# Performance work log

Hardware: AMD Instinct MI355X
Metric: run time of the kernel (lower is better)

The kernel has to match this reference:

```python
import jax, jax.numpy as jnp
import numpy as np

# SMPL-style 22-joint kinematic tree; parents[i] < i for i >= 2 as the module's loop requires.
PARENTS = np.array([-1, 0, 0, 0, 1, 2, 3, 4, 5, 6, 7, 8, 9, 9, 9, 12, 13, 14, 16, 17, 18, 19])
L, J, D6 = 65536, 22, 6


def cont6d_to_mat(d6):
    """6D continuous rotation -> 3x3 rotation matrix (Gram-Schmidt). Columns are b1,b2,b3."""
    a1, a2 = d6[..., :3], d6[..., 3:]
    b1 = a1 / jnp.maximum(jnp.linalg.norm(a1, axis=-1, keepdims=True), 1e-12)
    b2 = a2 - b1 * jnp.sum(b1 * a2, axis=-1, keepdims=True)
    b2 = b2 / jnp.maximum(jnp.linalg.norm(b2, axis=-1, keepdims=True), 1e-12)
    b3 = jnp.cross(b1, b2)
    return jnp.stack((b1, b2, b3), axis=-1)  # (..., 3, 3)


def setup_inputs() -> dict:
    key = jax.random.key(0)
    k1, k2 = jax.random.split(key)
    pred_series = jax.random.normal(k1, (L, J, D6), dtype=jnp.float32)
    offsets = 0.1 * jax.random.normal(k2, (J, 3), dtype=jnp.float32)  # bone offsets (buffer)
    return {"pred_series": pred_series, "offsets": offsets}


def reference(pred_series, offsets):
    # pred_series: (L, 22, 6) -> global positions (L, 22, 3)
    rot_mats = cont6d_to_mat(pred_series)          # (L, 22, 3, 3)

    # Cumulative root rotation: R_t = R_{t-1} @ delta_t, R_{-1} = I  (sequential scan over time)
    deltas = rot_mats[:, 1]                        # (L, 3, 3)
    def step(R, d):
        Rn = R @ d
        return Rn, Rn
    _, R = jax.lax.scan(step, jnp.eye(3, dtype=pred_series.dtype), deltas)  # (L, 3, 3)

    # Root translation: integrate rotated local velocities
    vel_local = pred_series[:, 0, :3]              # (L, 3)
    global_vel = jnp.einsum('tij,tj->ti', R, vel_local)
    root_pos = jnp.cumsum(global_vel, axis=0)      # (L, 3)

    # FK down the static tree, vectorized over time; unrolled over 22 joints (static).
    rots = [None] * J
    pos = [None] * J
    rots[0], pos[0] = R, root_pos
    rots[1] = R
    pos[1] = pos[0] + jnp.einsum('tij,j->ti', R, offsets[1])
    for i in range(2, J):
        p = int(PARENTS[i])
        rots[i] = jnp.einsum('tij,tjk->tik', rots[p], rot_mats[:, i])
        pos[i] = pos[p] + jnp.einsum('tij,j->ti', rots[p], offsets[i])
    return jnp.stack(pos, axis=1)                  # (L, 22, 3)
```

## Files before the change

### kernel.cpp

```cpp
#include <hip/hip_runtime.h>
#include <stdint.h>


#define LTOT 65536
#define ROW 132
#define P1B 256
#define NBLK (LTOT / P1B)

struct Aff { float A[9]; float b[3]; };

__device__ __forceinline__ void d6_to_mat(float a0, float a1, float a2,
                                          float a3, float a4, float a5,
                                          float R[9]) {
  float n1 = sqrtf(a0 * a0 + a1 * a1 + a2 * a2);
  float i1 = 1.0f / fmaxf(n1, 1e-12f);
  float b10 = a0 * i1, b11 = a1 * i1, b12 = a2 * i1;
  float d = b10 * a3 + b11 * a4 + b12 * a5;
  float c0 = a3 - d * b10, c1 = a4 - d * b11, c2 = a5 - d * b12;
  float n2 = sqrtf(c0 * c0 + c1 * c1 + c2 * c2);
  float i2 = 1.0f / fmaxf(n2, 1e-12f);
  float b20 = c0 * i2, b21 = c1 * i2, b22 = c2 * i2;
  float b30 = b11 * b22 - b12 * b21;
  float b31 = b12 * b20 - b10 * b22;
  float b32 = b10 * b21 - b11 * b20;
  R[0] = b10; R[1] = b20; R[2] = b30;
  R[3] = b11; R[4] = b21; R[5] = b31;
  R[6] = b12; R[7] = b22; R[8] = b32;
}

__device__ __forceinline__ void mat_mul(const float A[9], const float B[9], float C[9]) {
#pragma unroll
  for (int i = 0; i < 3; ++i)
#pragma unroll
    for (int j = 0; j < 3; ++j)
      C[i * 3 + j] = A[i * 3 + 0] * B[0 + j] + A[i * 3 + 1] * B[3 + j] + A[i * 3 + 2] * B[6 + j];
}

__device__ __forceinline__ void mat_vec(const float A[9], float x, float y, float z,
                                        float& ox, float& oy, float& oz) {
  ox = A[0] * x + A[1] * y + A[2] * z;
  oy = A[3] * x + A[4] * y + A[5] * z;
  oz = A[6] * x + A[7] * y + A[8] * z;
}

__device__ __forceinline__ void compose(const Aff& P, const Aff& T, Aff& O) {
  mat_mul(P.A, T.A, O.A);
  float bx, by, bz;
  mat_vec(P.A, T.b[0], T.b[1], T.b[2], bx, by, bz);
  O.b[0] = P.b[0] + bx; O.b[1] = P.b[1] + by; O.b[2] = P.b[2] + bz;
}

__device__ __forceinline__ void aff_identity(Aff& v) {
  v.A[0] = 1.f; v.A[1] = 0.f; v.A[2] = 0.f;
  v.A[3] = 0.f; v.A[4] = 1.f; v.A[5] = 0.f;
  v.A[6] = 0.f; v.A[7] = 0.f; v.A[8] = 1.f;
  v.b[0] = 0.f; v.b[1] = 0.f; v.b[2] = 0.f;
}

__device__ __forceinline__ void wave_scan(Aff& v, int lane) {
#pragma unroll
  for (int s = 1; s < 64; s <<= 1) {
    Aff u;
#pragma unroll
    for (int k = 0; k < 9; ++k) u.A[k] = __shfl_up(v.A[k], s, 64);
#pragma unroll
    for (int k = 0; k < 3; ++k) u.b[k] = __shfl_up(v.b[k], s, 64);
    if (lane >= s) { Aff t; compose(u, v, t); v = t; }
  }
}

__device__ __forceinline__ void block_scan(Aff& v, int lane, int wid,
                                           float (*sagg)[12], Aff& f) {
  wave_scan(v, lane);
  if (lane == 63) {
#pragma unroll
    for (int k = 0; k < 9; ++k) sagg[wid][k] = v.A[k];
#pragma unroll
    for (int k = 0; k < 3; ++k) sagg[wid][9 + k] = v.b[k];
  }
  __syncthreads();
  Aff pre; aff_identity(pre);
  for (int w = 0; w < wid; ++w) {
    Aff g, t2;
#pragma unroll
    for (int k = 0; k < 9; ++k) g.A[k] = sagg[w][k];
#pragma unroll
    for (int k = 0; k < 3; ++k) g.b[k] = sagg[w][9 + k];
    compose(pre, g, t2); pre = t2;
  }
  compose(pre, v, f);
}

__device__ __forceinline__ void elem_transform(const float* __restrict__ pred,
                                               int t, Aff& v) {
  const float4* q4 = (const float4*)(pred + (size_t)t * ROW);
  float4 qa = q4[0];
  float4 qb = q4[1];
  float4 qc = q4[2];
  d6_to_mat(qb.z, qb.w, qc.x, qc.y, qc.z, qc.w, v.A);
  mat_vec(v.A, qa.x, qa.y, qa.z, v.b[0], v.b[1], v.b[2]);
}

__global__ __launch_bounds__(P1B) void fk_agg(const float* __restrict__ pred,
                                              float* __restrict__ agg) {
  int tid = threadIdx.x;
  int t = blockIdx.x * P1B + tid;
  int lane = tid & 63, wid = tid >> 6;
  Aff v;
  elem_transform(pred, t, v);
  wave_scan(v, lane);
  __shared__ float sagg[P1B / 64][12];
  if (lane == 63) {
#pragma unroll
    for (int k = 0; k < 9; ++k) sagg[wid][k] = v.A[k];
#pragma unroll
    for (int k = 0; k < 3; ++k) sagg[wid][9 + k] = v.b[k];
  }
  __syncthreads();
  if (tid == P1B - 1) {
    Aff pre; aff_identity(pre);
    for (int w = 0; w < P1B / 64 - 1; ++w) {
      Aff g, t2;
#pragma unroll
      for (int k = 0; k < 9; ++k) g.A[k] = sagg[w][k];
#pragma unroll
      for (int k = 0; k < 3; ++k) g.b[k] = sagg[w][9 + k];
      compose(pre, g, t2); pre = t2;
    }
    Aff f; compose(pre, v, f);
    float4* a = (float4*)(agg + (size_t)blockIdx.x * 12);
    a[0] = make_float4(f.A[0], f.A[1], f.A[2], f.A[3]);
    a[1] = make_float4(f.A[4], f.A[5], f.A[6], f.A[7]);
    a[2] = make_float4(f.A[8], f.b[0], f.b[1], f.b[2]);
  }
}

__global__ __launch_bounds__(P1B) void fk_main(const float* __restrict__ pred,
                                               const float* __restrict__ offs,
                                               const float* __restrict__ agg,
                                               float* __restrict__ out) {
  int tid = threadIdx.x;
  int t = blockIdx.x * P1B + tid;
  int lane = tid & 63, wid = tid >> 6;

  __shared__ float sagg1[P1B / 64][12];
  __shared__ float sagg2[P1B / 64][12];
  __shared__ float sincl[NBLK][13];

  Aff v2;
  {
    const float4* a = (const float4*)(agg + (size_t)tid * 12);
    float4 a0 = a[0], a1 = a[1], a2 = a[2];
    v2.A[0] = a0.x; v2.A[1] = a0.y; v2.A[2] = a0.z; v2.A[3] = a0.w;
    v2.A[4] = a1.x; v2.A[5] = a1.y; v2.A[6] = a1.z; v2.A[7] = a1.w;
    v2.A[8] = a2.x; v2.b[0] = a2.y; v2.b[1] = a2.z; v2.b[2] = a2.w;
  }

  Aff v, f;
  elem_transform(pred, t, v);
  block_scan(v, lane, wid, sagg1, f);

  Aff incl;
  block_scan(v2, lane, wid, sagg2, incl);
#pragma unroll
  for (int k = 0; k < 9; ++k) sincl[tid][k] = incl.A[k];
#pragma unroll
  for (int k = 0; k < 3; ++k) sincl[tid][9 + k] = incl.b[k];
  __syncthreads();

  Aff eb;
  if (blockIdx.x == 0) {
    aff_identity(eb);
  } else {
    const float* sp = sincl[blockIdx.x - 1];
#pragma unroll
    for (int k = 0; k < 9; ++k) eb.A[k] = sp[k];
#pragma unroll
    for (int k = 0; k < 3; ++k) eb.b[k] = sp[9 + k];
  }

  Aff g;
  compose(eb, f, g);
  const float* R = g.A;
  float ov[66];
  ov[0] = g.b[0]; ov[1] = g.b[1]; ov[2] = g.b[2];

  const float* q = pred + (size_t)t * ROW;

#define CHILD(j, p, Rp)                                                        \
  {                                                                            \
    float ox, oy, oz;                                                          \
    mat_vec(Rp, offs[(j)*3 + 0], offs[(j)*3 + 1], offs[(j)*3 + 2], ox, oy, oz);\
    ov[(j)*3 + 0] = ov[(p)*3 + 0] + ox;                                        \
    ov[(j)*3 + 1] = ov[(p)*3 + 1] + oy;                                        \
    ov[(j)*3 + 2] = ov[(p)*3 + 2] + oz;                                        \
  }
#define ROTJ(j, Rp, Rj)                                                        \
  {                                                                            \
    const float2* qq = (const float2*)(q + (j)*6);             \
    float2 w0 = qq[0], w1 = qq[1], w2 = qq[2];                                 \
    float Mx[9];                                                               \
    d6_to_mat(w0.x, w0.y, w1.x, w1.y, w2.x, w2.y, Mx);                         \
    mat_mul(Rp, Mx, Rj);                                                       \
  }

  CHILD(1, 0, R);
  float r2[9], r3[9], r4[9];
  CHILD(2, 0, R); ROTJ(2, R, r2);
  CHILD(3, 0, R); ROTJ(3, R, r3);
  CHILD(4, 1, R); ROTJ(4, R, r4);
  float r5[9], r6[9], r7[9];
  CHILD(5, 2, r2); ROTJ(5, r2, r5);
  CHILD(6, 3, r3); ROTJ(6, r3, r6);
  CHILD(7, 4, r4); ROTJ(7, r4, r7);
  float r8[9], r9[9];
  CHILD(8, 5, r5); ROTJ(8, r5, r8);
  CHILD(9, 6, r6); ROTJ(9, r6, r9);
  CHILD(10, 7, r7);
  CHILD(11, 8, r8);
  float r12[9], r13[9], r14[9];
  CHILD(12, 9, r9); ROTJ(12, r9, r12);
  CHILD(13, 9, r9); ROTJ(13, r9, r13);
  CHILD(14, 9, r9); ROTJ(14, r9, r14);
  CHILD(15, 12, r12);
  float r16[9], r17[9];
  CHILD(16, 13, r13); ROTJ(16, r13, r16);
  CHILD(17, 14, r14); ROTJ(17, r14, r17);
  float r18[9], r19[9];
  CHILD(18, 16, r16); ROTJ(18, r16, r18);
  CHILD(19, 17, r17); ROTJ(19, r17, r19);
  CHILD(20, 18, r18);
  CHILD(21, 19, r19);

  float2* ob = (float2*)(out + (size_t)t * 66);
#pragma unroll
  for (int k = 0; k < 33; ++k) ob[k] = make_float2(ov[2 * k], ov[2 * k + 1]);
#undef CHILD
#undef ROTJ
}

extern "C" void kernel_launch(void* const* d_in, const int* in_sizes, int n_in,
                              void* d_out, int out_size, void* d_ws, size_t ws_size,
                              hipStream_t stream) {
  const float* pred = (const float*)d_in[0];
  const float* offs = (const float*)d_in[1];
  float* out = (float*)d_out;
  float* agg = (float*)d_ws;

  fk_agg<<<NBLK, P1B, 0, stream>>>(pred, agg);
  fk_main<<<NBLK, P1B, 0, stream>>>(pred, offs, agg, out);
}
```

Before: 95.63 us.

## Split joint-tree FK across four waves per time block and stage output in LDS

The first kernel now computes the full block-local scan of root transforms and writes per-timestep prefixes to workspace, so the second kernel no longer redoes that scan. The second kernel processes 64 timesteps per 256-thread block and splits the kinematic tree into four branches, one per wave, to raise parallelism and reduce per-thread register pressure. Joint positions are staged in shared memory and written out with coalesced float4 stores. The cost is an extra 48 bytes per timestep written and read through global memory, recomputation of shared ancestor chains in several waves, and a redundant block-aggregate scan in each of the four times more blocks.

```diff
diff --git a/kernel.cpp b/kernel.cpp
--- a/kernel.cpp
+++ b/kernel.cpp
@@ -6,8 +6,11 @@
 #define ROW 132
 #define P1B 256
 #define NBLK (LTOT / P1B)
+#define TB 64
+#define NTB (LTOT / TB)
 
 struct Aff { float A[9]; float b[3]; };
+struct V3 { float x, y, z; };
 
 __device__ __forceinline__ void d6_to_mat(float a0, float a1, float a2,
                                           float a3, float a4, float a5,
@@ -101,33 +104,46 @@
   mat_vec(v.A, qa.x, qa.y, qa.z, v.b[0], v.b[1], v.b[2]);
 }
 
-__global__ __launch_bounds__(P1B) void fk_agg(const float* __restrict__ pred,
-                                              float* __restrict__ agg) {
+__device__ __forceinline__ void rotj(const float* __restrict__ q, int j,
+                                     const float Rp[9], float Rj[9]) {
+  const float2* qq = (const float2*)(q + j * 6);
+  float2 w0 = qq[0], w1 = qq[1], w2 = qq[2];
+  float Mx[9];
+  d6_to_mat(w0.x, w0.y, w1.x, w1.y, w2.x, w2.y, Mx);
+  mat_mul(Rp, Mx, Rj);
+}
+
+__device__ __forceinline__ V3 childpos(const float* __restrict__ offs, int j,
+                                       V3 pp, const float Rp[9]) {
+  float ox, oy, oz;
+  mat_vec(Rp, offs[j * 3 + 0], offs[j * 3 + 1], offs[j * 3 + 2], ox, oy, oz);
+  V3 r; r.x = pp.x + ox; r.y = pp.y + oy; r.z = pp.z + oz; return r;
+}
+
+__device__ __forceinline__ void stp(float (*spos)[66], int lane, int j, V3 p) {
+  spos[lane][j * 3 + 0] = p.x;
+  spos[lane][j * 3 + 1] = p.y;
+  spos[lane][j * 3 + 2] = p.z;
+}
+
+__global__ __launch_bounds__(P1B) void fk_scan(const float* __restrict__ pred,
+                                               float* __restrict__ agg,
+                                               float* __restrict__ floc) {
   int tid = threadIdx.x;
   int t = blockIdx.x * P1B + tid;
   int lane = tid & 63, wid = tid >> 6;
-  Aff v;
+  __shared__ float sagg[P1B / 64][12];
+
+  Aff v, f;
   elem_transform(pred, t, v);
-  wave_scan(v, lane);
-  __shared__ float sagg[P1B / 64][12];
-  if (lane == 63) {
-#pragma unroll
-    for (int k = 0; k < 9; ++k) sagg[wid][k] = v.A[k];
-#pragma unroll
-    for (int k = 0; k < 3; ++k) sagg[wid][9 + k] = v.b[k];
-  }
-  __syncthreads();
+  block_scan(v, lane, wid, sagg, f);
+
+  float4* fp = (float4*)(floc + (size_t)t * 12);
+  fp[0] = make_float4(f.A[0], f.A[1], f.A[2], f.A[3]);
+  fp[1] = make_float4(f.A[4], f.A[5], f.A[6], f.A[7]);
+  fp[2] = make_float4(f.A[8], f.b[0], f.b[1], f.b[2]);
+
   if (tid == P1B - 1) {
-    Aff pre; aff_identity(pre);
-    for (int w = 0; w < P1B / 64 - 1; ++w) {
-      Aff g, t2;
-#pragma unroll
-      for (int k = 0; k < 9; ++k) g.A[k] = sagg[w][k];
-#pragma unroll
-      for (int k = 0; k < 3; ++k) g.b[k] = sagg[w][9 + k];
-      compose(pre, g, t2); pre = t2;
-    }
-    Aff f; compose(pre, v, f);
     float4* a = (float4*)(agg + (size_t)blockIdx.x * 12);
     a[0] = make_float4(f.A[0], f.A[1], f.A[2], f.A[3]);
     a[1] = make_float4(f.A[4], f.A[5], f.A[6], f.A[7]);
@@ -135,17 +151,27 @@
   }
 }
 
-__global__ __launch_bounds__(P1B) void fk_main(const float* __restrict__ pred,
-                                               const float* __restrict__ offs,
-                                               const float* __restrict__ agg,
-                                               float* __restrict__ out) {
+__global__ __launch_bounds__(P1B, 4) void fk_tree(const float* __restrict__ pred,
+                                                  const float* __restrict__ offs,
+                                                  const float* __restrict__ agg,
+                                                  const float* __restrict__ floc,
+                                                  float* __restrict__ out) {
   int tid = threadIdx.x;
-  int t = blockIdx.x * P1B + tid;
   int lane = tid & 63, wid = tid >> 6;
-
-  __shared__ float sagg1[P1B / 64][12];
-  __shared__ float sagg2[P1B / 64][12];
-  __shared__ float sincl[NBLK][13];
+  int t = blockIdx.x * TB + lane;
+
+  __shared__ float sagg[P1B / 64][12];
+  __shared__ float ebs[12];
+  __shared__ __align__(16) float spos[TB][66];
+
+  Aff fv;
+  {
+    const float4* fp = (const float4*)(floc + (size_t)t * 12);
+    float4 a0 = fp[0], a1 = fp[1], a2 = fp[2];
+    fv.A[0] = a0.x; fv.A[1] = a0.y; fv.A[2] = a0.z; fv.A[3] = a0.w;
+    fv.A[4] = a1.x; fv.A[5] = a1.y; fv.A[6] = a1.z; fv.A[7] = a1.w;
+    fv.A[8] = a2.x; fv.b[0] = a2.y; fv.b[1] = a2.z; fv.b[2] = a2.w;
+  }
 
   Aff v2;
   {
@@ -155,88 +181,93 @@
     v2.A[4] = a1.x; v2.A[5] = a1.y; v2.A[6] = a1.z; v2.A[7] = a1.w;
     v2.A[8] = a2.x; v2.b[0] = a2.y; v2.b[1] = a2.z; v2.b[2] = a2.w;
   }
-
-  Aff v, f;
-  elem_transform(pred, t, v);
-  block_scan(v, lane, wid, sagg1, f);
-
   Aff incl;
-  block_scan(v2, lane, wid, sagg2, incl);
-#pragma unroll
-  for (int k = 0; k < 9; ++k) sincl[tid][k] = incl.A[k];
-#pragma unroll
-  for (int k = 0; k < 3; ++k) sincl[tid][9 + k] = incl.b[k];
+  block_scan(v2, lane, wid, sagg, incl);
+
+  int tb = blockIdx.x >> 2;
+  if (tid == tb - 1) {
+#pragma unroll
+    for (int k = 0; k < 9; ++k) ebs[k] = incl.A[k];
+#pragma unroll
+    for (int k = 0; k < 3; ++k) ebs[9 + k] = incl.b[k];
+  }
   __syncthreads();
 
   Aff eb;
-  if (blockIdx.x == 0) {
+  if (tb == 0) {
     aff_identity(eb);
   } else {
-    const float* sp = sincl[blockIdx.x - 1];
-#pragma unroll
-    for (int k = 0; k < 9; ++k) eb.A[k] = sp[k];
-#pragma unroll
-    for (int k = 0; k < 3; ++k) eb.b[k] = sp[9 + k];
-  }
-
-  Aff g;
-  compose(eb, f, g);
+#pragma unroll
+    for (int k = 0; k < 9; ++k) eb.A[k] = ebs[k];
+#pragma unroll
+    for (int k = 0; k < 3; ++k) eb.b[k] = ebs[9 + k];
+  }
+
+  Aff g; compose(eb, fv, g);
   const float* R = g.A;
-  float ov[66];
-  ov[0] = g.b[0]; ov[1] = g.b[1]; ov[2] = g.b[2];
-
+  V3 p0; p0.x = g.b[0]; p0.y = g.b[1]; p0.z = g.b[2];
   const float* q = pred + (size_t)t * ROW;
 
-#define CHILD(j, p, Rp)                                                        \
-  {                                                                            \
-    float ox, oy, oz;                                                          \
-    mat_vec(Rp, offs[(j)*3 + 0], offs[(j)*3 + 1], offs[(j)*3 + 2], ox, oy, oz);\
-    ov[(j)*3 + 0] = ov[(p)*3 + 0] + ox;                                        \
-    ov[(j)*3 + 1] = ov[(p)*3 + 1] + oy;                                        \
-    ov[(j)*3 + 2] = ov[(p)*3 + 2] + oz;                                        \
-  }
-#define ROTJ(j, Rp, Rj)                                                        \
-  {                                                                            \
-    const float2* qq = (const float2*)(q + (j)*6);             \
-    float2 w0 = qq[0], w1 = qq[1], w2 = qq[2];                                 \
-    float Mx[9];                                                               \
-    d6_to_mat(w0.x, w0.y, w1.x, w1.y, w2.x, w2.y, Mx);                         \
-    mat_mul(Rp, Mx, Rj);                                                       \
-  }
-
-  CHILD(1, 0, R);
-  float r2[9], r3[9], r4[9];
-  CHILD(2, 0, R); ROTJ(2, R, r2);
-  CHILD(3, 0, R); ROTJ(3, R, r3);
-  CHILD(4, 1, R); ROTJ(4, R, r4);
-  float r5[9], r6[9], r7[9];
-  CHILD(5, 2, r2); ROTJ(5, r2, r5);
-  CHILD(6, 3, r3); ROTJ(6, r3, r6);
-  CHILD(7, 4, r4); ROTJ(7, r4, r7);
-  float r8[9], r9[9];
-  CHILD(8, 5, r5); ROTJ(8, r5, r8);
-  CHILD(9, 6, r6); ROTJ(9, r6, r9);
-  CHILD(10, 7, r7);
-  CHILD(11, 8, r8);
-  float r12[9], r13[9], r14[9];
-  CHILD(12, 9, r9); ROTJ(12, r9, r12);
-  CHILD(13, 9, r9); ROTJ(13, r9, r13);
-  CHILD(14, 9, r9); ROTJ(14, r9, r14);
-  CHILD(15, 12, r12);
-  float r16[9], r17[9];
-  CHILD(16, 13, r13); ROTJ(16, r13, r16);
-  CHILD(17, 14, r14); ROTJ(17, r14, r17);
-  float r18[9], r19[9];
-  CHILD(18, 16, r16); ROTJ(18, r16, r18);
-  CHILD(19, 17, r17); ROTJ(19, r17, r19);
-  CHILD(20, 18, r18);
-  CHILD(21, 19, r19);
-
-  float2* ob = (float2*)(out + (size_t)t * 66);
-#pragma unroll
-  for (int k = 0; k < 33; ++k) ob[k] = make_float2(ov[2 * k], ov[2 * k + 1]);
-#undef CHILD
-#undef ROTJ
+  if (wid == 0) {
+    stp(spos, lane, 0, p0);
+    V3 p1 = childpos(offs, 1, p0, R);  stp(spos, lane, 1, p1);
+    V3 p2 = childpos(offs, 2, p0, R);  stp(spos, lane, 2, p2);
+    float r2[9]; rotj(q, 2, R, r2);
+    V3 p5 = childpos(offs, 5, p2, r2); stp(spos, lane, 5, p5);
+    float r5[9]; rotj(q, 5, r2, r5);
+    V3 p8 = childpos(offs, 8, p5, r5); stp(spos, lane, 8, p8);
+    float r8[9]; rotj(q, 8, r5, r8);
+    V3 p11 = childpos(offs, 11, p8, r8); stp(spos, lane, 11, p11);
+  } else if (wid == 1) {
+    V3 p1 = childpos(offs, 1, p0, R);
+    V3 p4 = childpos(offs, 4, p1, R);  stp(spos, lane, 4, p4);
+    float r4[9]; rotj(q, 4, R, r4);
+    V3 p7 = childpos(offs, 7, p4, r4); stp(spos, lane, 7, p7);
+    float r7[9]; rotj(q, 7, r4, r7);
+    V3 p10 = childpos(offs, 10, p7, r7); stp(spos, lane, 10, p10);
+    V3 p3 = childpos(offs, 3, p0, R);  stp(spos, lane, 3, p3);
+    float r3[9]; rotj(q, 3, R, r3);
+    V3 p6 = childpos(offs, 6, p3, r3); stp(spos, lane, 6, p6);
+    float r6[9]; rotj(q, 6, r3, r6);
+    V3 p9 = childpos(offs, 9, p6, r6); stp(spos, lane, 9, p9);
+    float r9[9]; rotj(q, 9, r6, r9);
+    V3 p12 = childpos(offs, 12, p9, r9); stp(spos, lane, 12, p12);
+    float r12[9]; rotj(q, 12, r9, r12);
+    V3 p15 = childpos(offs, 15, p12, r12); stp(spos, lane, 15, p15);
+  } else {
+    V3 p3 = childpos(offs, 3, p0, R);
+    float r3[9]; rotj(q, 3, R, r3);
+    V3 p6 = childpos(offs, 6, p3, r3);
+    float r6[9]; rotj(q, 6, r3, r6);
+    V3 p9 = childpos(offs, 9, p6, r6);
+    float r9[9]; rotj(q, 9, r6, r9);
+    if (wid == 2) {
+      V3 p13 = childpos(offs, 13, p9, r9); stp(spos, lane, 13, p13);
+      float r13[9]; rotj(q, 13, r9, r13);
+      V3 p16 = childpos(offs, 16, p13, r13); stp(spos, lane, 16, p16);
+      float r16[9]; rotj(q, 16, r13, r16);
+      V3 p18 = childpos(offs, 18, p16, r16); stp(spos, lane, 18, p18);
+      float r18[9]; rotj(q, 18, r16, r18);
+      V3 p20 = childpos(offs, 20, p18, r18); stp(spos, lane, 20, p20);
+    } else {
+      V3 p14 = childpos(offs, 14, p9, r9); stp(spos, lane, 14, p14);
+      float r14[9]; rotj(q, 14, r9, r14);
+      V3 p17 = childpos(offs, 17, p14, r14); stp(spos, lane, 17, p17);
+      float r17[9]; rotj(q, 17, r14, r17);
+      V3 p19 = childpos(offs, 19, p17, r17); stp(spos, lane, 19, p19);
+      float r19[9]; rotj(q, 19, r17, r19);
+      V3 p21 = childpos(offs, 21, p19, r19); stp(spos, lane, 21, p21);
+    }
+  }
+
+  __syncthreads();
+  const float4* sp = (const float4*)&spos[0][0];
+  float4* op = (float4*)(out + (size_t)blockIdx.x * TB * 66);
+#pragma unroll
+  for (int k = 0; k < (TB * 66 / 4 + P1B - 1) / P1B; ++k) {
+    int idx = tid + k * P1B;
+    if (idx < TB * 66 / 4) op[idx] = sp[idx];
+  }
 }
 
 extern "C" void kernel_launch(void* const* d_in, const int* in_sizes, int n_in,
@@ -246,7 +277,8 @@
   const float* offs = (const float*)d_in[1];
   float* out = (float*)d_out;
   float* agg = (float*)d_ws;
-
-  fk_agg<<<NBLK, P1B, 0, stream>>>(pred, agg);
-  fk_main<<<NBLK, P1B, 0, stream>>>(pred, offs, agg, out);
-}
+  float* floc = (float*)((char*)d_ws + 16384);
+
+  fk_scan<<<NBLK, P1B, 0, stream>>>(pred, agg, floc);
+  fk_tree<<<NTB, P1B, 0, stream>>>(pred, offs, agg, floc, out);
+}
```

After: 90.24 us. -5.6%, faster.
